# Performance work log

Hardware: AMD Instinct MI355X
Metric: run time of the kernel (lower is better)

## Reference

```python
import jax, jax.numpy as jnp
import numpy as np

D_INPUT = 1024
N_HEADS = 16
D_INNER = 64
SEQ = 1024
PREV = 1024
BS = 4
LN_EPS = 1e-5


def _rel_shift(x):
    # x: (i, j, b, h) -> Transformer-XL relative shift trick
    i, j, b, h = x.shape
    zero_pad = jnp.zeros((i, 1, b, h), dtype=x.dtype)
    return jnp.concatenate([zero_pad, x], axis=1).reshape(j + 1, i, b, h)[1:].reshape(i, j, b, h)


def setup_inputs() -> dict:
    key = jax.random.key(0)
    ks = jax.random.split(key, 9)
    w = 0.02
    return {
        "input_": jax.random.normal(ks[0], (SEQ, BS, D_INPUT), jnp.float32),
        "pos_embs": jax.random.normal(ks[1], (SEQ + PREV, D_INPUT), jnp.float32),
        "memory": jax.random.normal(ks[2], (PREV, BS, D_INPUT), jnp.float32),
        "u": jax.random.normal(ks[3], (N_HEADS, D_INNER), jnp.float32) * w,
        "v": jax.random.normal(ks[4], (N_HEADS, D_INNER), jnp.float32) * w,
        "W_kv": jax.random.normal(ks[5], (D_INPUT, 2 * N_HEADS * D_INNER), jnp.float32) * w,
        "W_q": jax.random.normal(ks[6], (D_INPUT, N_HEADS * D_INNER), jnp.float32) * w,
        "W_p": jax.random.normal(ks[7], (D_INPUT, N_HEADS * D_INNER), jnp.float32) * w,
        "W_out": jax.random.normal(ks[8], (N_HEADS * D_INNER, D_INPUT), jnp.float32) * w,
        "ln_g": jnp.ones((D_INPUT,), jnp.float32),
        "ln_b": jnp.zeros((D_INPUT,), jnp.float32),
    }


def reference(input_, pos_embs, memory, u, v, W_kv, W_q, W_p, W_out, ln_g, ln_b):
    S, B, D = input_.shape
    P = memory.shape[0]
    T = S + P
    H, d = u.shape
    scale = 1.0 / (d ** 0.5)

    x_mem = jnp.concatenate([memory, input_], axis=0)          # (T, B, D)
    kv = x_mem @ W_kv                                          # (T, B, 2*H*d)
    k, val = jnp.split(kv, 2, axis=-1)
    k = k.reshape(T, B, H, d)
    val = val.reshape(T, B, H, d)
    q = (input_ @ W_q).reshape(S, B, H, d)                     # (S, B, H, d)

    content_attn = jnp.einsum('ibhd,jbhd->ijbh', q + u, k)     # (S, T, B, H)
    p = (pos_embs @ W_p).reshape(T, H, d)                      # (T, H, d)
    position_attn = jnp.einsum('ibhd,jhd->ijbh', q + v, p)     # (S, T, B, H)
    position_attn = _rel_shift(position_attn)

    attn = jax.nn.softmax((content_attn + position_attn) * scale, axis=1)
    awv = jnp.einsum('ijbh,jbhd->ibhd', attn, val).reshape(S, B, H * d)

    out = input_ + awv @ W_out                                 # residual
    mu = jnp.mean(out, axis=-1, keepdims=True)
    var = jnp.mean(jnp.square(out - mu), axis=-1, keepdims=True)
    return (out - mu) * jax.lax.rsqrt(var + LN_EPS) * ln_g + ln_b
```

## Files before the change

### kernel.cpp

```cpp
#include <hip/hip_runtime.h>
#include <cstdint>
#include <cstddef>

#define S_  1024
#define B_  4
#define T_  2048
#define H_  16

typedef short     short8 __attribute__((ext_vector_type(8)));
typedef float     f32x4  __attribute__((ext_vector_type(4)));
typedef unsigned short u16x8 __attribute__((ext_vector_type(8)));

__device__ __forceinline__ unsigned short f2b(float f){
  uint32_t x = __builtin_bit_cast(uint32_t, f);
  x = (x + 0x7fffu + ((x >> 16) & 1u)) >> 16;
  return (unsigned short)x;
}
__device__ __forceinline__ unsigned short f2bt(float f){
  return (unsigned short)(__builtin_bit_cast(uint32_t, f) >> 16);
}
__device__ __forceinline__ float b2f(unsigned short u){
  return __builtin_bit_cast(float, ((uint32_t)u) << 16);
}

__device__ __forceinline__ void gl_lds16(const unsigned short* g, unsigned short* l){
  __builtin_amdgcn_global_load_lds(
      (const __attribute__((address_space(1))) void*)g,
      (__attribute__((address_space(3))) void*)l,
      16, 0, 0);
}

__global__ __launch_bounds__(256) void cvt_all(
    const float* __restrict__ memsrc, const float* __restrict__ inp,
    const float* __restrict__ pos,
    unsigned short* __restrict__ xb, unsigned short* __restrict__ posb)
{
  int i = (blockIdx.x * 256 + threadIdx.x) * 4;
  const float* src;
  unsigned short* dst;
  if (i < 8192 * 1024){
    src = (i < 4096 * 1024) ? (memsrc + i) : (inp + (i - 4096 * 1024));
    dst = xb + i;
  } else {
    int i2 = i - 8192 * 1024;
    src = pos + i2;
    dst = posb + i2;
  }
  float4 x = *(const float4*)src;
  ushort4 o;
  o.x = f2b(x.x); o.y = f2b(x.y); o.z = f2b(x.z); o.w = f2b(x.w);
  *(ushort4*)dst = o;
}

__global__ __launch_bounds__(256) void wtrans_all(
    const float* __restrict__ Wkv, const float* __restrict__ Wq,
    const float* __restrict__ Wp,  const float* __restrict__ Wout,
    unsigned short* __restrict__ WkvT, unsigned short* __restrict__ WqT,
    unsigned short* __restrict__ WpT,  unsigned short* __restrict__ WoutT)
{
  __shared__ float tile[32][33];
  int blk = blockIdx.x;
  const float* in; unsigned short* out; int C, bx, by;
  if (blk < 2048){ in = Wkv; out = WkvT; C = 2048; bx = blk & 63; by = blk >> 6; }
  else {
    int r = blk - 2048; int wi = r >> 10; r &= 1023;
    C = 1024; bx = r & 31; by = r >> 5;
    in  = (wi == 0) ? Wq  : ((wi == 1) ? Wp  : Wout);
    out = (wi == 0) ? WqT : ((wi == 1) ? WpT : WoutT);
  }
  const int R0 = by * 32, C0 = bx * 32;
  const int t = threadIdx.x;
  const int r = t >> 3, c4 = (t & 7) * 4;
  float4 x = *(const float4*)(in + (size_t)(R0 + r) * C + C0 + c4);
  tile[r][c4+0] = x.x; tile[r][c4+1] = x.y; tile[r][c4+2] = x.z; tile[r][c4+3] = x.w;
  __syncthreads();
  ushort4 o;
  o.x = f2b(tile[c4+0][r]); o.y = f2b(tile[c4+1][r]);
  o.z = f2b(tile[c4+2][r]); o.w = f2b(tile[c4+3][r]);
  *(ushort4*)(out + (size_t)(C0 + r) * 1024 + R0 + c4) = o;
}

__global__ __launch_bounds__(256) void vtrans(
    const unsigned short* __restrict__ kvb, unsigned short* __restrict__ vtg)
{
  __shared__ __align__(16) unsigned short tile[64][72];
  const int t = threadIdx.x;
  const int bh = blockIdx.y;
  const int b = bh >> 4, h = bh & 15;
  const int t0 = blockIdx.x * 64;
  #pragma unroll
  for (int l = 0; l < 2; ++l){
    int idx = t + l * 256;
    int row = idx >> 3, seg = (idx & 7) * 8;
    u16x8 x = *(const u16x8*)(kvb + ((size_t)(t0 + row) * 4 + b) * 2048 + 1024 + h * 64 + seg);
    *(u16x8*)&tile[row][seg] = x;
  }
  __syncthreads();
  #pragma unroll
  for (int l = 0; l < 2; ++l){
    int idx = t + l * 256;
    int d = idx >> 3, nseg = (idx & 7) * 8;
    u16x8 o;
    #pragma unroll
    for (int j = 0; j < 8; ++j) o[j] = tile[nseg + j][d];
    *(u16x8*)(vtg + ((size_t)bh * 64 + d) * 2048 + t0 + nseg) = o;
  }
}

#define AS_IDX(row,k) ((((row) >> 3) * 512) + (((k) >> 3) * 64) + (((row) & 7) * 8) + ((k) & 7))

__global__ __launch_bounds__(256) void gemm_multi(
    const unsigned short* __restrict__ xb,
    const unsigned short* __restrict__ posb,
    const unsigned short* __restrict__ WkvT,
    const unsigned short* __restrict__ WqT,
    const unsigned short* __restrict__ WpT,
    unsigned short* __restrict__ kvb,
    unsigned short* __restrict__ qbb,
    unsigned short* __restrict__ pbb)
{
  const unsigned short *A, *BT;
  unsigned short* C;
  int N, local;
  int bx = (blockIdx.x & 7) * 176 + (blockIdx.x >> 3);
  if (bx < 1024){       A = xb;                       BT = WkvT; C = kvb; N = 2048; local = bx;        }
  else if (bx < 1280){  A = xb + (size_t)4096 * 1024; BT = WqT;  C = qbb; N = 1024; local = bx - 1024; }
  else {                A = posb;                     BT = WpT;  C = pbb; N = 1024; local = bx - 1280; }
  const int nb = N >> 7;
  const int M0 = (local / nb) * 128, N0 = (local % nb) * 128;
  const int K = 1024;

  __shared__ __align__(16) unsigned short As[128 * 64];
  __shared__ __align__(16) unsigned short Bs[128 * 64];
  const int t = threadIdx.x;
  const int w = t >> 6, lane = t & 63, quad = lane >> 4, l16 = lane & 15;
  const int wm = (w >> 1) * 64, wn = (w & 1) * 64;
  const int lr = lane & 7, lcb = lane >> 3;

  f32x4 acc[4][4] = {};

  for (int k0 = 0; k0 < K; k0 += 64){
    __syncthreads();
    #pragma unroll
    for (int i = 0; i < 4; ++i){
      int blk = 4 * w + i;
      gl_lds16(A  + (size_t)(M0 + 8 * blk + lr) * K + k0 + lcb * 8, As + blk * 512);
      gl_lds16(BT + (size_t)(N0 + 8 * blk + lr) * K + k0 + lcb * 8, Bs + blk * 512);
    }
    __syncthreads();
    #pragma unroll
    for (int ks = 0; ks < 2; ++ks){
      short8 af[4], bf[4];
      #pragma unroll
      for (int rt = 0; rt < 4; ++rt)
        af[rt] = *(short8*)&As[AS_IDX(wm + rt * 16 + l16, ks * 32 + quad * 8)];
      #pragma unroll
      for (int ct = 0; ct < 4; ++ct)
        bf[ct] = *(short8*)&Bs[AS_IDX(wn + ct * 16 + l16, ks * 32 + quad * 8)];
      #pragma unroll
      for (int rt = 0; rt < 4; ++rt)
        #pragma unroll
        for (int ct = 0; ct < 4; ++ct)
          acc[rt][ct] = __builtin_amdgcn_mfma_f32_16x16x32_bf16(af[rt], bf[ct], acc[rt][ct], 0, 0, 0);
    }
  }

  #pragma unroll
  for (int rt = 0; rt < 4; ++rt)
    #pragma unroll
    for (int r = 0; r < 4; ++r){
      int row = M0 + wm + rt * 16 + quad * 4 + r;
      #pragma unroll
      for (int ct = 0; ct < 4; ++ct)
        C[(size_t)row * N + N0 + wn + ct * 16 + l16] = f2b(acc[rt][ct][r]);
    }
}

__global__ __launch_bounds__(256) void gemm_outk(
    const unsigned short* __restrict__ A,
    const unsigned short* __restrict__ BT,
    float* __restrict__ OutP)
{
  const int K = 1024, N = 1024;
  int lid = blockIdx.x + 8 * (blockIdx.y + 32 * blockIdx.z);
  int sw  = (lid & 7) * 64 + (lid >> 3);
  const int N0 = (sw & 7) * 128;
  const int M0 = ((sw >> 3) & 31) * 128;
  const int kz = sw >> 8;
  const int k0s = kz * 512, k0e = k0s + 512;
  float* outF = OutP + (size_t)kz * 4096 * 1024;

  __shared__ __align__(16) unsigned short As[128 * 64];
  __shared__ __align__(16) unsigned short Bs[128 * 64];
  const int t = threadIdx.x;
  const int w = t >> 6, lane = t & 63, quad = lane >> 4, l16 = lane & 15;
  const int wm = (w >> 1) * 64, wn = (w & 1) * 64;
  const int lr = lane & 7, lcb = lane >> 3;

  f32x4 acc[4][4] = {};

  for (int k0 = k0s; k0 < k0e; k0 += 64){
    __syncthreads();
    #pragma unroll
    for (int i = 0; i < 4; ++i){
      int blk = 4 * w + i;
      gl_lds16(A  + (size_t)(M0 + 8 * blk + lr) * K + k0 + lcb * 8, As + blk * 512);
      gl_lds16(BT + (size_t)(N0 + 8 * blk + lr) * K + k0 + lcb * 8, Bs + blk * 512);
    }
    __syncthreads();
    #pragma unroll
    for (int ks = 0; ks < 2; ++ks){
      short8 af[4], bf[4];
      #pragma unroll
      for (int rt = 0; rt < 4; ++rt)
        af[rt] = *(short8*)&As[AS_IDX(wm + rt * 16 + l16, ks * 32 + quad * 8)];
      #pragma unroll
      for (int ct = 0; ct < 4; ++ct)
        bf[ct] = *(short8*)&Bs[AS_IDX(wn + ct * 16 + l16, ks * 32 + quad * 8)];
      #pragma unroll
      for (int rt = 0; rt < 4; ++rt)
        #pragma unroll
        for (int ct = 0; ct < 4; ++ct)
          acc[rt][ct] = __builtin_amdgcn_mfma_f32_16x16x32_bf16(af[rt], bf[ct], acc[rt][ct], 0, 0, 0);
    }
  }

  #pragma unroll
  for (int rt = 0; rt < 4; ++rt)
    #pragma unroll
    for (int r = 0; r < 4; ++r){
      int row = M0 + wm + rt * 16 + quad * 4 + r;
      #pragma unroll
      for (int ct = 0; ct < 4; ++ct)
        outF[(size_t)row * N + N0 + wn + ct * 16 + l16] = acc[rt][ct][r];
    }
}

#define SP_IX(gm,n) ((gm) * 64 + ((n) ^ (((gm) & 12) << 2)))

__global__ __launch_bounds__(256, 3) void attn_mfma(
    const unsigned short* __restrict__ qb,
    const unsigned short* __restrict__ kvb,
    const unsigned short* __restrict__ pbm,
    const unsigned short* __restrict__ vtg,
    const float* __restrict__ ub, const float* __restrict__ vb,
    unsigned short* __restrict__ awvb)
{
  __shared__ __align__(16) unsigned short Kc[64 * 64];
  __shared__ __align__(16) unsigned short VT[64 * 64];
  __shared__ __align__(16) unsigned short Pw[128 * 64];
  __shared__ __align__(16) unsigned short SP[64 * 64];

  const int t = threadIdx.x;
  const int i0 = blockIdx.x * 64;
  const int bh = blockIdx.y;
  const int b = bh >> 4, h = bh & 15;
  const int w = t >> 6, lane = t & 63, quad = lane >> 4, l16 = lane & 15;
  const int colbase = h * 64 + quad * 8;
  const int ctLo = 3 - w;

  const float SCQ = 0.1803368801f;
  const float EOF_ = 23.0831206f;

  short8 qu[2], qv[2][2];
  #pragma unroll
  for (int cs = 0; cs < 2; ++cs){
    int gr = i0 + 16 * w + l16 + cs;
    #pragma unroll
    for (int ks = 0; ks < 2; ++ks){
      u16x8 q8 = *(const u16x8*)(qb + ((size_t)gr * 4 + b) * 1024 + colbase + ks * 32);
      #pragma unroll
      for (int j = 0; j < 8; ++j){
        float f = b2f(q8[j]);
        qv[cs][ks][j] = (short)f2b((f + vb[colbase + ks * 32 + j]) * SCQ);
        if (cs == 0) qu[ks][j] = (short)f2b((f + ub[colbase + ks * 32 + j]) * SCQ);
      }
    }
  }

  f32x4 oacc[4] = {};
  float lsum[4] = {0.f, 0.f, 0.f, 0.f};

  u16x8 pk[2], pv2[2], pp[4];

  auto loadKV = [&](int jc){
    const int j0 = jc * 64;
    #pragma unroll
    for (int l = 0; l < 2; ++l){
      int idx = t + l * 256;
      int row = idx >> 3, cb = idx & 7;
      pk[l]  = *(const u16x8*)(kvb + ((size_t)(j0 + row) * 4 + b) * 2048 + h * 64 + cb * 8);
      pv2[l] = *(const u16x8*)(vtg + ((size_t)bh * 64 + row) * 2048 + j0 + cb * 8);
    }
  };

  auto loadPPfull = [&](int jc){
    const int D = jc * 64 - i0;
    #pragma unroll
    for (int l = 0; l < 4; ++l){
      int idx = t + l * 256;
      int row = idx >> 3, cb = idx & 7;
      int pr;
      if (D <= 960)          pr = D + 960 + row;
      else if (D == 1024)    pr = (row < 64) ? (1984 + row) : (row - 65);
      else                   pr = D - 1089 + row;
      u16x8 x;
      if (pr >= 0 && pr < T_){
        x = *(const u16x8*)(pbm + (size_t)pr * 1024 + h * 64 + cb * 8);
      } else {
        for (int j = 0; j < 8; ++j) x[j] = 0;
      }
      pp[l] = x;
    }
  };

  auto loadPPhalf = [&](int jc){
    const int D = jc * 64 - i0;
    #pragma unroll
    for (int l = 0; l < 2; ++l){
      int idx = t + l * 256;
      int rowh = idx >> 3, cb = idx & 7;
      int pr = (D <= 960) ? (D + 1024 + rowh) : (D - 1025 + rowh);
      u16x8 x;
      if (pr >= 0 && pr < T_){
        x = *(const u16x8*)(pbm + (size_t)pr * 1024 + h * 64 + cb * 8);
      } else {
        for (int j = 0; j < 8; ++j) x[j] = 0;
      }
      pp[l] = x;
    }
  };

  auto storeKV = [&](){
    #pragma unroll
    for (int l = 0; l < 2; ++l){
      int idx = t + l * 256;
      int row = idx >> 3, cb = idx & 7;
      int sw = (cb ^ (row & 7)) * 8;
      *(u16x8*)&Kc[row * 64 + sw] = pk[l];
      *(u16x8*)&VT[row * 64 + sw] = pv2[l];
    }
  };
  auto storePPfull = [&](){
    #pragma unroll
    for (int l = 0; l < 4; ++l){
      int idx = t + l * 256;
      int row = idx >> 3, cb = idx & 7;
      *(u16x8*)&Pw[row * 64 + ((cb ^ (row & 7)) * 8)] = pp[l];
    }
  };
  auto storePPhalf = [&](int physh){
    #pragma unroll
    for (int l = 0; l < 2; ++l){
      int idx = t + l * 256;
      int rowh = idx >> 3, cb = idx & 7;
      *(u16x8*)&Pw[(physh * 64 + rowh) * 64 + ((cb ^ (rowh & 7)) * 8)] = pp[l];
    }
  };

  loadKV(0);
  loadPPfull(0);
  int par = 0;

  #pragma unroll 1
  for (int jc = 0; jc < 32; ++jc){
    const int D = jc * 64 - i0;

    __syncthreads();
    storeKV();
    if (jc == 0) storePPfull(); else storePPhalf(1 ^ par);
    if (jc + 1 < 32){ loadKV(jc + 1); loadPPhalf(jc + 1); }
    __syncthreads();

    #pragma unroll
    for (int ci = 0; ci < 5; ++ci){
      int ct = ctLo + ci;
      int cs = (D <= 960) ? 0 : ((D >= 1088) ? 1 : ((ct >= 4) ? 1 : 0));
      f32x4 racc = {};
      #pragma unroll
      for (int ks = 0; ks < 2; ++ks){
        int rr = ct * 16 + l16;
        int prow = ((rr >> 6) ^ par) * 64 + (rr & 63);
        short8 bf = *(short8*)&Pw[prow * 64 + (((ks * 4 + quad) ^ (rr & 7)) * 8)];
        racc = __builtin_amdgcn_mfma_f32_16x16x32_bf16(qv[cs][ks], bf, racc, 0, 0, 0);
      }
      int c = ct * 16 + l16;
      #pragma unroll
      for (int r = 0; r < 4; ++r){
        int gm = 16 * w + quad * 4 + r;
        int n = c + gm - 63;
        if ((unsigned)n < 64u) SP[SP_IX(gm, n)] = f2bt(racc[r]);
      }
    }

    f32x4 cacc[4] = {};
    #pragma unroll
    for (int ks = 0; ks < 2; ++ks){
      #pragma unroll
      for (int ct = 0; ct < 4; ++ct){
        int rr = ct * 16 + l16;
        short8 bf = *(short8*)&Kc[rr * 64 + (((ks * 4 + quad) ^ (rr & 7)) * 8)];
        cacc[ct] = __builtin_amdgcn_mfma_f32_16x16x32_bf16(qu[ks], bf, cacc[ct], 0, 0, 0);
      }
    }

    #pragma unroll
    for (int ct = 0; ct < 4; ++ct){
      #pragma unroll
      for (int r = 0; r < 4; ++r){
        int gm = 16 * w + quad * 4 + r;
        int n = ct * 16 + l16;
        int ix = SP_IX(gm, n);
        float s = cacc[ct][r] + b2f(SP[ix]);
        float e = __builtin_amdgcn_exp2f(s - EOF_);
        lsum[r] += e;
        SP[ix] = f2bt(e);
      }
    }

    #pragma unroll
    for (int ks = 0; ks < 2; ++ks){
      short8 af = *(short8*)&SP[SP_IX(16 * w + l16, ks * 32 + quad * 8)];
      #pragma unroll
      for (int dt = 0; dt < 4; ++dt){
        int rr = dt * 16 + l16;
        short8 bf = *(short8*)&VT[rr * 64 + (((ks * 4 + quad) ^ (rr & 7)) * 8)];
        oacc[dt] = __builtin_amdgcn_mfma_f32_16x16x32_bf16(af, bf, oacc[dt], 0, 0, 0);
      }
    }

    par ^= 1;
  }

  #pragma unroll
  for (int r = 0; r < 4; ++r){
    float red = lsum[r];
    #pragma unroll
    for (int mk = 1; mk < 16; mk <<= 1)
      red += __shfl_xor(red, mk, 64);
    float inv = 1.f / red;
    int srow = i0 + 16 * w + quad * 4 + r;
    int grow = srow * 4 + b;
    #pragma unroll
    for (int dt = 0; dt < 4; ++dt)
      awvb[(size_t)grow * 1024 + h * 64 + dt * 16 + l16] = f2bt(oacc[dt][r] * inv);
  }
}

__global__ __launch_bounds__(256) void ln2_kernel(
    const float* __restrict__ inp, const float* __restrict__ OutP,
    const float* __restrict__ g, const float* __restrict__ bb,
    float* __restrict__ out)
{
  const int row = blockIdx.x, t = threadIdx.x;
  float4 x  = *(const float4*)(inp  + (size_t)row * 1024 + t * 4);
  float4 p0 = *(const float4*)(OutP + (size_t)row * 1024 + t * 4);
  float4 p1 = *(const float4*)(OutP + (size_t)4096 * 1024 + row * 1024 + t * 4);
  x.x += p0.x + p1.x; x.y += p0.y + p1.y; x.z += p0.z + p1.z; x.w += p0.w + p1.w;
  float s  = x.x + x.y + x.z + x.w;
  float s2 = x.x*x.x + x.y*x.y + x.z*x.z + x.w*x.w;
  #pragma unroll
  for (int o = 32; o > 0; o >>= 1){
    s  += __shfl_down(s, o);
    s2 += __shfl_down(s2, o);
  }
  __shared__ float rs[4], rs2[4];
  int w = t >> 6, lane = t & 63;
  if (lane == 0){ rs[w] = s; rs2[w] = s2; }
  __syncthreads();
  s  = rs[0] + rs[1] + rs[2] + rs[3];
  s2 = rs2[0] + rs2[1] + rs2[2] + rs2[3];
  float mu   = s * (1.f/1024.f);
  float var  = s2 * (1.f/1024.f) - mu*mu;
  float rstd = rsqrtf(var + 1e-5f);
  float4 gg = *(const float4*)(g + t*4);
  float4 bv = *(const float4*)(bb + t*4);
  float4 o;
  o.x = (x.x - mu)*rstd*gg.x + bv.x;
  o.y = (x.y - mu)*rstd*gg.y + bv.y;
  o.z = (x.z - mu)*rstd*gg.z + bv.z;
  o.w = (x.w - mu)*rstd*gg.w + bv.w;
  *(float4*)(out + (size_t)row * 1024 + t * 4) = o;
}

extern "C" void kernel_launch(void* const* d_in, const int* in_sizes, int n_in,
                              void* d_out, int out_size, void* d_ws, size_t ws_size,
                              hipStream_t stream) {
  (void)in_sizes; (void)n_in; (void)out_size; (void)ws_size;
  const float* input_ = (const float*)d_in[0];
  const float* pos    = (const float*)d_in[1];
  const float* mem    = (const float*)d_in[2];
  const float* u      = (const float*)d_in[3];
  const float* v      = (const float*)d_in[4];
  const float* Wkv    = (const float*)d_in[5];
  const float* Wq     = (const float*)d_in[6];
  const float* Wp     = (const float*)d_in[7];
  const float* Wout   = (const float*)d_in[8];
  const float* lng    = (const float*)d_in[9];
  const float* lnb    = (const float*)d_in[10];
  float* out = (float*)d_out;

  unsigned short* ws   = (unsigned short*)d_ws;
  unsigned short* xb    = ws;
  unsigned short* posb  = xb    + (size_t)8192*1024;
  unsigned short* WkvT  = posb  + (size_t)2048*1024;
  unsigned short* WqT   = WkvT  + (size_t)2048*1024;
  unsigned short* WpT   = WqT   + (size_t)1024*1024;
  unsigned short* WoutT = WpT   + (size_t)1024*1024;
  unsigned short* kvb   = WoutT + (size_t)1024*1024;
  unsigned short* qbb   = kvb   + (size_t)8192*2048;
  unsigned short* pbb   = qbb   + (size_t)4096*1024;
  unsigned short* vtg   = pbb   + (size_t)2048*1024;
  unsigned short* awvb  = vtg   + (size_t)4096*2048;

  float* OutP = (float*)kvb;

  cvt_all<<<10240, 256, 0, stream>>>(mem, input_, pos, xb, posb);
  wtrans_all<<<5120, 256, 0, stream>>>(Wkv, Wq, Wp, Wout, WkvT, WqT, WpT, WoutT);

  gemm_multi<<<1408, 256, 0, stream>>>(xb, posb, WkvT, WqT, WpT, kvb, qbb, pbb);

  vtrans<<<dim3(32, 64), 256, 0, stream>>>(kvb, vtg);

  attn_mfma<<<dim3(16, 64), 256, 0, stream>>>(qbb, kvb, pbb, vtg, u, v, awvb);

  gemm_outk<<<dim3(8, 32, 2), 256, 0, stream>>>(awvb, WoutT, OutP);
  ln2_kernel<<<4096, 256, 0, stream>>>(input_, OutP, lng, lnb, out);
}
```

Measured before the change: 414.1 us.

## Split attention key range in two and add a partial-sum combine kernel

Launches the attention kernel with a third grid dimension that splits the 32 key chunks into two halves of 16. Each half writes unnormalized bf16 output partials and per-row softmax denominators into reused workspace buffers. A new combine kernel adds the two partials, divides by the summed denominator and writes the final bf16 attention output. The aim is to double the number of blocks, reducing the tail imbalance of 1024 blocks at 3 per CU. The cost is an extra launch, extra global traffic for the partials, and an additional bf16 truncation of unnormalized values. The partials can be summed directly because the softmax uses a fixed exponent offset rather than a running max.

New measurement: 403.3 us. -2.6%, faster.

```diff
diff --git a/kernel.cpp b/kernel.cpp
--- a/kernel.cpp
+++ b/kernel.cpp
@@ -244,7 +244,8 @@
     const unsigned short* __restrict__ pbm,
     const unsigned short* __restrict__ vtg,
     const float* __restrict__ ub, const float* __restrict__ vb,
-    unsigned short* __restrict__ awvb)
+    unsigned short* __restrict__ opart,
+    float* __restrict__ lpart)
 {
   __shared__ __align__(16) unsigned short Kc[64 * 64];
   __shared__ __align__(16) unsigned short VT[64 * 64];
@@ -254,6 +255,7 @@
   const int t = threadIdx.x;
   const int i0 = blockIdx.x * 64;
   const int bh = blockIdx.y;
+  const int jh = blockIdx.z;
   const int b = bh >> 4, h = bh & 15;
   const int w = t >> 6, lane = t & 63, quad = lane >> 4, l16 = lane & 15;
   const int colbase = h * 64 + quad * 8;
@@ -358,18 +360,19 @@
     }
   };
 
-  loadKV(0);
-  loadPPfull(0);
+  const int jcs = jh * 16, jce = jcs + 16;
+  loadKV(jcs);
+  loadPPfull(jcs);
   int par = 0;
 
   #pragma unroll 1
-  for (int jc = 0; jc < 32; ++jc){
+  for (int jc = jcs; jc < jce; ++jc){
     const int D = jc * 64 - i0;
 
     __syncthreads();
     storeKV();
-    if (jc == 0) storePPfull(); else storePPhalf(1 ^ par);
-    if (jc + 1 < 32){ loadKV(jc + 1); loadPPhalf(jc + 1); }
+    if (jc == jcs) storePPfull(); else storePPhalf(1 ^ par);
+    if (jc + 1 < jce){ loadKV(jc + 1); loadPPhalf(jc + 1); }
     __syncthreads();
 
     #pragma unroll
@@ -432,19 +435,39 @@
     par ^= 1;
   }
 
+  unsigned short* ob = opart + (size_t)jh * 4096 * 1024;
+  float* lb = lpart + (size_t)jh * 4096 * 16;
   #pragma unroll
   for (int r = 0; r < 4; ++r){
     float red = lsum[r];
     #pragma unroll
     for (int mk = 1; mk < 16; mk <<= 1)
       red += __shfl_xor(red, mk, 64);
-    float inv = 1.f / red;
     int srow = i0 + 16 * w + quad * 4 + r;
     int grow = srow * 4 + b;
     #pragma unroll
     for (int dt = 0; dt < 4; ++dt)
-      awvb[(size_t)grow * 1024 + h * 64 + dt * 16 + l16] = f2bt(oacc[dt][r] * inv);
-  }
+      ob[(size_t)grow * 1024 + h * 64 + dt * 16 + l16] = f2bt(oacc[dt][r]);
+    if (l16 == 0) lb[(size_t)grow * 16 + h] = red;
+  }
+}
+
+__global__ __launch_bounds__(256) void attn_combine(
+    const unsigned short* __restrict__ opart, const float* __restrict__ lpart,
+    unsigned short* __restrict__ awvb)
+{
+  const int grow = blockIdx.x, t = threadIdx.x;
+  const int d4 = t * 4, h = t >> 4;
+  float l = lpart[(size_t)grow * 16 + h] + lpart[(size_t)4096 * 16 + grow * 16 + h];
+  float inv = 1.f / l;
+  ushort4 a = *(const ushort4*)(opart + (size_t)grow * 1024 + d4);
+  ushort4 c = *(const ushort4*)(opart + (size_t)4096 * 1024 + grow * 1024 + d4);
+  ushort4 o;
+  o.x = f2bt((b2f(a.x) + b2f(c.x)) * inv);
+  o.y = f2bt((b2f(a.y) + b2f(c.y)) * inv);
+  o.z = f2bt((b2f(a.z) + b2f(c.z)) * inv);
+  o.w = f2bt((b2f(a.w) + b2f(c.w)) * inv);
+  *(ushort4*)(awvb + (size_t)grow * 1024 + d4) = o;
 }
 
 __global__ __launch_bounds__(256) void ln2_kernel(
@@ -513,7 +536,9 @@
   unsigned short* vtg   = pbb   + (size_t)2048*1024;
   unsigned short* awvb  = vtg   + (size_t)4096*2048;
 
-  float* OutP = (float*)kvb;
+  unsigned short* opart = xb;
+  float*          lpart = (float*)posb;
+  float*          OutP  = (float*)kvb;
 
   cvt_all<<<10240, 256, 0, stream>>>(mem, input_, pos, xb, posb);
   wtrans_all<<<5120, 256, 0, stream>>>(Wkv, Wq, Wp, Wout, WkvT, WqT, WpT, WoutT);
@@ -522,7 +547,8 @@
 
   vtrans<<<dim3(32, 64), 256, 0, stream>>>(kvb, vtg);
 
-  attn_mfma<<<dim3(16, 64), 256, 0, stream>>>(qbb, kvb, pbb, vtg, u, v, awvb);
+  attn_mfma<<<dim3(16, 64, 2), 256, 0, stream>>>(qbb, kvb, pbb, vtg, u, v, opart, lpart);
+  attn_combine<<<4096, 256, 0, stream>>>(opart, lpart, awvb);
 
   gemm_outk<<<dim3(8, 32, 2), 256, 0, stream>>>(awvb, WoutT, OutP);
   ln2_kernel<<<4096, 256, 0, stream>>>(input_, OutP, lng, lnb, out);
```
